# Performance work log

Measured on AMD Instinct MI355X. Metric: run time of the kernel, lower is better.

The kernel has to match this reference:

```python
import jax, jax.numpy as jnp
import numpy as np

BATCH, INPUT_DIM, HIDDEN_DIM, SEQ_LENGTH = 128, 256, 512, 1024


def setup_inputs() -> dict:
    key = jax.random.key(0)
    k1, k2, k3, k4, k5 = jax.random.split(key, 5)
    s = 1.0 / np.sqrt(HIDDEN_DIM)  # PyTorch GRU init: U(-1/sqrt(H), 1/sqrt(H))
    return {
        "input_features": jax.random.normal(k1, (BATCH, INPUT_DIM), dtype=jnp.float32),
        # PyTorch layout: rows stacked as [reset; update; new], each [H, *]
        "w_ih": jax.random.uniform(k2, (3 * HIDDEN_DIM, INPUT_DIM), minval=-s, maxval=s, dtype=jnp.float32),
        "w_hh": jax.random.uniform(k3, (3 * HIDDEN_DIM, HIDDEN_DIM), minval=-s, maxval=s, dtype=jnp.float32),
        "b_ih": jax.random.uniform(k4, (3 * HIDDEN_DIM,), minval=-s, maxval=s, dtype=jnp.float32),
        "b_hh": jax.random.uniform(k5, (3 * HIDDEN_DIM,), minval=-s, maxval=s, dtype=jnp.float32),
    }


def reference(input_features, w_ih, w_hh, b_ih, b_hh):
    # Decoder: run the GRU cell SEQ_LENGTH times with the SAME input x each
    # step, feeding back the hidden state; collect per-step outputs.
    B = input_features.shape[0]
    H = w_hh.shape[1]
    # Input contribution is constant across steps -> compute once.  [B, 3H]
    gi = input_features @ w_ih.T + b_ih
    gi_r, gi_z, gi_n = jnp.split(gi, 3, axis=-1)

    def step(h, _):
        gh = h @ w_hh.T + b_hh  # [B, 3H]
        gh_r, gh_z, gh_n = jnp.split(gh, 3, axis=-1)
        r = jax.nn.sigmoid(gi_r + gh_r)
        z = jax.nn.sigmoid(gi_z + gh_z)
        n = jnp.tanh(gi_n + r * gh_n)
        h_new = (1.0 - z) * n + z * h
        return h_new, h_new

    h0 = jnp.zeros((B, H), dtype=input_features.dtype)
    _, outs = jax.lax.scan(step, h0, None, length=SEQ_LENGTH)  # [S, B, H]
    return jnp.transpose(outs, (1, 0, 2))  # [B, SEQ_LENGTH, H]
```

## Files before the change

### kernel.cpp

```cpp
#include <hip/hip_runtime.h>
#include <hip/hip_bf16.h>
#include <stdint.h>


constexpr int SEQ = 1024;
constexpr int BATCH = 128;
constexpr int IND = 256;
constexpr int HD = 512;
constexpr int BG = 8;
constexpr int HG = 32;
constexpr int ROWS = BATCH / BG;
constexpr int NT = 3;
constexpr int RING_D = 8;
constexpr int SLOT_DW = BATCH * HD / 2;
constexpr size_t RING_BYTES = (size_t)RING_D * SLOT_DW * 4;

using frag16 = __attribute__((ext_vector_type(8))) short;
using f32x4  = __attribute__((ext_vector_type(4))) float;
using u32x4  = __attribute__((ext_vector_type(4))) unsigned;

__device__ __forceinline__ float sigmoid_f(float x) {
    return 1.f / (1.f + __expf(-x));
}
__device__ __forceinline__ float tanh_f(float x) {
    float e = __expf(2.f * x);
    return 1.f - 2.f / (e + 1.f);
}
__device__ __forceinline__ short f2bf(float x) {
    return (short)__bfloat16_as_ushort(__float2bfloat16(x));
}

__global__ __launch_bounds__(64, 1) void gru_kernel(
    const float* __restrict__ x,
    const float* __restrict__ w_ih,
    const float* __restrict__ w_hh,
    const float* __restrict__ b_ih,
    const float* __restrict__ b_hh,
    unsigned* __restrict__ ring,
    float* __restrict__ out)
{
    const int lane = threadIdx.x;
    const int bg = blockIdx.x & 7;
    const int hg = blockIdx.x >> 3;
    const int b0 = bg * ROWS;
    const int c0 = hg * 16;
    const int nlo = lane & 15;
    const int quad = lane >> 4;

    int gcol[NT];
    gcol[0] = c0 + nlo;
    gcol[1] = HD + c0 + nlo;
    gcol[2] = 2 * HD + c0 + nlo;

    __shared__ frag16 ldsB[NT * 16 * 64];
#pragma unroll
    for (int t = 0; t < NT; ++t) {
        for (int kc = 0; kc < 16; ++kc) {
            const float* src = w_hh + (size_t)gcol[t] * HD + kc * 32 + quad * 8;
            float4 v0 = *(const float4*)src;
            float4 v1 = *(const float4*)(src + 4);
            frag16 f;
            f[0] = f2bf(v0.x); f[1] = f2bf(v0.y); f[2] = f2bf(v0.z); f[3] = f2bf(v0.w);
            f[4] = f2bf(v1.x); f[5] = f2bf(v1.y); f[6] = f2bf(v1.z); f[7] = f2bf(v1.w);
            ldsB[(t * 16 + kc) * 64 + lane] = f;
        }
    }

    float gi[NT][4];
    float bhn = b_hh[gcol[2]];
#pragma unroll
    for (int t = 0; t < NT; ++t) {
        float bi = b_ih[gcol[t]] + ((t < 2) ? b_hh[gcol[t]] : 0.f);
#pragma unroll
        for (int r = 0; r < 4; ++r) gi[t][r] = bi;
    }
    for (int r = 0; r < 4; ++r) {
        const float4* xr = (const float4*)(x + (size_t)(b0 + quad * 4 + r) * IND);
        for (int kc = 0; kc < IND / 4; ++kc) {
            float4 xv = xr[kc];
#pragma unroll
            for (int t = 0; t < NT; ++t) {
                float4 wv = ((const float4*)(w_ih + (size_t)gcol[t] * IND))[kc];
                gi[t][r] += xv.x * wv.x + xv.y * wv.y + xv.z * wv.z + xv.w * wv.w;
            }
        }
    }

    const size_t arow_byte = (size_t)(b0 + nlo) * (HD * 2) + quad * 16;

    float hreg[4] = {0.f, 0.f, 0.f, 0.f};

    for (int s = 0; s < SEQ; ++s) {
        f32x4 C[NT];
#pragma unroll
        for (int t = 0; t < NT; ++t) C[t] = (f32x4){0.f, 0.f, 0.f, 0.f};

        if (s > 0) {
            const char* lrow =
                (const char*)(ring + ((s - 1) & (RING_D - 1)) * SLOT_DW) + arow_byte;
            u32x4 raw[16];
            unsigned vmask = 0u;
            do {
#pragma unroll
                for (int kc = 0; kc < 16; ++kc) {
                    if (!(vmask & (1u << kc))) {
                        asm volatile("global_load_dwordx4 %0, %1, off sc0 sc1"
                                     : "=v"(raw[kc]) : "v"(lrow + kc * 64) : "memory");
                    }
                }
                asm volatile("s_waitcnt vmcnt(0)" ::: "memory");
                __builtin_amdgcn_sched_barrier(0);
#pragma unroll
                for (int kc = 0; kc < 16; ++kc) {
                    if (!(vmask & (1u << kc))) {
                        unsigned orr = raw[kc][0] | raw[kc][1] | raw[kc][2] | raw[kc][3];
                        if (__ballot((orr & 0x40004000u) == 0u) == ~0ull)
                            vmask |= (1u << kc);
                    }
                }
            } while (vmask != 0xFFFFu);
#pragma unroll
            for (int kc = 0; kc < 16; ++kc) {
                union { u32x4 u; frag16 f; } cv;
                cv.u = raw[kc];
#pragma unroll
                for (int t = 0; t < NT; ++t) {
                    frag16 bfr = ldsB[(t * 16 + kc) * 64 + lane];
                    C[t] = __builtin_amdgcn_mfma_f32_16x16x32_bf16(cv.f, bfr, C[t], 0, 0, 0);
                }
            }
        }

        unsigned* wslot = ring + (s & (RING_D - 1)) * SLOT_DW;
        unsigned* rslot = ring + ((s + 2) & (RING_D - 1)) * SLOT_DW;
        float hn[4];
#pragma unroll
        for (int r = 0; r < 4; ++r) {
            float gr  = gi[0][r] + C[0][r];
            float gz  = gi[1][r] + C[1][r];
            float ghn = C[2][r] + bhn;
            float rr = sigmoid_f(gr);
            float zz = sigmoid_f(gz);
            float nn = tanh_f(gi[2][r] + rr * ghn);
            hn[r] = (1.f - zz) * nn + zz * hreg[r];
            hreg[r] = hn[r];
            unsigned own = (unsigned)(unsigned short)f2bf(hn[r]);
            unsigned other = (unsigned)__shfl_xor((int)own, 1);
            if ((lane & 1) == 0) {
                int row = b0 + quad * 4 + r;
                unsigned idx = (unsigned)(row * HD + (c0 + nlo)) >> 1;
                __hip_atomic_store(wslot + idx, own | (other << 16),
                                   __ATOMIC_RELAXED, __HIP_MEMORY_SCOPE_SYSTEM);
            }
        }
#pragma unroll
        for (int r = 0; r < 4; ++r) {
            if ((lane & 1) == 0) {
                int row = b0 + quad * 4 + r;
                unsigned idx = (unsigned)(row * HD + (c0 + nlo)) >> 1;
                __hip_atomic_store(rslot + idx, 0xFFFFFFFFu,
                                   __ATOMIC_RELAXED, __HIP_MEMORY_SCOPE_SYSTEM);
            }
        }
#pragma unroll
        for (int r = 0; r < 4; ++r) {
            int row = b0 + quad * 4 + r;
            __builtin_nontemporal_store(
                hn[r], out + (size_t)row * (SEQ * HD) + (size_t)s * HD + (c0 + nlo));
        }
    }
}

extern "C" void kernel_launch(void* const* d_in, const int* in_sizes, int n_in,
                              void* d_out, int out_size, void* d_ws, size_t ws_size,
                              hipStream_t stream) {
    (void)in_sizes; (void)n_in; (void)out_size; (void)ws_size;
    const float* x    = (const float*)d_in[0];
    const float* w_ih = (const float*)d_in[1];
    const float* w_hh = (const float*)d_in[2];
    const float* b_ih = (const float*)d_in[3];
    const float* b_hh = (const float*)d_in[4];

    unsigned* ring = (unsigned*)d_ws;
    hipMemsetAsync(ring, 0xFF, RING_BYTES, stream);
    gru_kernel<<<BG * HG, 64, 0, stream>>>(x, w_ih, w_hh, b_ih, b_hh, ring,
                                           (float*)d_out);
}
```

Before: 2.974 ms.

## Overlap ring polling with MFMA and defer output/sentinel stores off critical path

Restructures the per-step spin-wait on the shared hidden-state ring. Loads are issued once up front, then each polled chunk that is ready is consumed immediately by its MFMAs while only the not-yet-ready chunks are reloaded. The sentinel reset of a future ring slot and the output store for the previous step move into the window where loads are in flight, taking them off the step's critical path. Readiness is combined with a shuffle-AND reduction instead of a ballot per chunk. The sentinel now resets slot s+1 rather than s+2, which narrows the margin against blocks that fall behind, and the extra bookkeeping adds to the polling loop.

```diff
diff --git a/kernel.cpp b/kernel.cpp
--- a/kernel.cpp
+++ b/kernel.cpp
@@ -99,41 +99,75 @@
             const char* lrow =
                 (const char*)(ring + ((s - 1) & (RING_D - 1)) * SLOT_DW) + arow_byte;
             u32x4 raw[16];
-            unsigned vmask = 0u;
+#pragma unroll
+            for (int kc = 0; kc < 16; ++kc)
+                asm volatile("global_load_dwordx4 %0, %1, off sc0 sc1"
+                             : "=&v"(raw[kc]) : "v"(lrow + kc * 64) : "memory");
+            {
+                unsigned* rslot = ring + ((s + 1) & (RING_D - 1)) * SLOT_DW;
+#pragma unroll
+                for (int r = 0; r < 4; ++r) {
+                    if ((lane & 1) == 0) {
+                        int row = b0 + quad * 4 + r;
+                        unsigned idx = (unsigned)(row * HD + (c0 + nlo)) >> 1;
+                        __hip_atomic_store(rslot + idx, 0xFFFFFFFFu,
+                                           __ATOMIC_RELAXED, __HIP_MEMORY_SCOPE_SYSTEM);
+                    }
+                }
+#pragma unroll
+                for (int r = 0; r < 4; ++r) {
+                    int row = b0 + quad * 4 + r;
+                    __builtin_nontemporal_store(
+                        hreg[r],
+                        out + (size_t)row * (SEQ * HD) + (size_t)(s - 1) * HD + (c0 + nlo));
+                }
+            }
+            unsigned vmask = 0;
+            int round = 0;
             do {
-#pragma unroll
-                for (int kc = 0; kc < 16; ++kc) {
-                    if (!(vmask & (1u << kc))) {
-                        asm volatile("global_load_dwordx4 %0, %1, off sc0 sc1"
-                                     : "=v"(raw[kc]) : "v"(lrow + kc * 64) : "memory");
-                    }
-                }
-                asm volatile("s_waitcnt vmcnt(0)" ::: "memory");
+                if (round == 0)
+                    asm volatile("s_waitcnt vmcnt(8)" ::: "memory");
+                else
+                    asm volatile("s_waitcnt vmcnt(0)" ::: "memory");
+                ++round;
                 __builtin_amdgcn_sched_barrier(0);
+                unsigned ok = 0;
 #pragma unroll
                 for (int kc = 0; kc < 16; ++kc) {
                     if (!(vmask & (1u << kc))) {
                         unsigned orr = raw[kc][0] | raw[kc][1] | raw[kc][2] | raw[kc][3];
-                        if (__ballot((orr & 0x40004000u) == 0u) == ~0ull)
-                            vmask |= (1u << kc);
+                        ok |= ((orr & 0x40004000u) == 0u) ? (1u << kc) : 0u;
                     }
                 }
+#pragma unroll
+                for (int d = 1; d < 64; d <<= 1)
+                    ok &= (unsigned)__shfl_xor((int)ok, d);
+                unsigned newv = __builtin_amdgcn_readfirstlane(ok & ~vmask) & 0xFFFFu;
+                unsigned still = 0xFFFFu & ~(vmask | newv);
+#pragma unroll
+                for (int kc = 0; kc < 16; ++kc) {
+                    if (still & (1u << kc))
+                        asm volatile("global_load_dwordx4 %0, %1, off sc0 sc1"
+                                     : "=&v"(raw[kc]) : "v"(lrow + kc * 64) : "memory");
+                }
+#pragma unroll
+                for (int kc = 0; kc < 16; ++kc) {
+                    if (newv & (1u << kc)) {
+                        union { u32x4 u; frag16 f; } cv;
+                        cv.u = raw[kc];
+#pragma unroll
+                        for (int t = 0; t < NT; ++t) {
+                            frag16 bfr = ldsB[(t * 16 + kc) * 64 + lane];
+                            C[t] = __builtin_amdgcn_mfma_f32_16x16x32_bf16(cv.f, bfr,
+                                                                           C[t], 0, 0, 0);
+                        }
+                    }
+                }
+                vmask |= newv;
             } while (vmask != 0xFFFFu);
-#pragma unroll
-            for (int kc = 0; kc < 16; ++kc) {
-                union { u32x4 u; frag16 f; } cv;
-                cv.u = raw[kc];
-#pragma unroll
-                for (int t = 0; t < NT; ++t) {
-                    frag16 bfr = ldsB[(t * 16 + kc) * 64 + lane];
-                    C[t] = __builtin_amdgcn_mfma_f32_16x16x32_bf16(cv.f, bfr, C[t], 0, 0, 0);
-                }
-            }
         }
 
         unsigned* wslot = ring + (s & (RING_D - 1)) * SLOT_DW;
-        unsigned* rslot = ring + ((s + 2) & (RING_D - 1)) * SLOT_DW;
-        float hn[4];
 #pragma unroll
         for (int r = 0; r < 4; ++r) {
             float gr  = gi[0][r] + C[0][r];
@@ -142,9 +176,9 @@
             float rr = sigmoid_f(gr);
             float zz = sigmoid_f(gz);
             float nn = tanh_f(gi[2][r] + rr * ghn);
-            hn[r] = (1.f - zz) * nn + zz * hreg[r];
-            hreg[r] = hn[r];
-            unsigned own = (unsigned)(unsigned short)f2bf(hn[r]);
+            float hn = (1.f - zz) * nn + zz * hreg[r];
+            hreg[r] = hn;
+            unsigned own = (unsigned)(unsigned short)f2bf(hn);
             unsigned other = (unsigned)__shfl_xor((int)own, 1);
             if ((lane & 1) == 0) {
                 int row = b0 + quad * 4 + r;
@@ -153,21 +187,14 @@
                                    __ATOMIC_RELAXED, __HIP_MEMORY_SCOPE_SYSTEM);
             }
         }
-#pragma unroll
-        for (int r = 0; r < 4; ++r) {
-            if ((lane & 1) == 0) {
-                int row = b0 + quad * 4 + r;
-                unsigned idx = (unsigned)(row * HD + (c0 + nlo)) >> 1;
-                __hip_atomic_store(rslot + idx, 0xFFFFFFFFu,
-                                   __ATOMIC_RELAXED, __HIP_MEMORY_SCOPE_SYSTEM);
-            }
-        }
-#pragma unroll
-        for (int r = 0; r < 4; ++r) {
-            int row = b0 + quad * 4 + r;
-            __builtin_nontemporal_store(
-                hn[r], out + (size_t)row * (SEQ * HD) + (size_t)s * HD + (c0 + nlo));
-        }
+    }
+
+#pragma unroll
+    for (int r = 0; r < 4; ++r) {
+        int row = b0 + quad * 4 + r;
+        __builtin_nontemporal_store(
+            hreg[r],
+            out + (size_t)row * (SEQ * HD) + (size_t)(SEQ - 1) * HD + (c0 + nlo));
     }
 }
 
```

Measured after the change: 5.366 ms. 1.8x slower.

## Pair two waves per block and share polled hidden-state halves through LDS

Applied to the files above, without the earlier changes.

Blocks now hold two wavefronts that cover adjacent 16-column slices. Each wave polls only half of the K chunks of the previous hidden state from the global ring and exchanges its half with the other wave through a double-buffered LDS buffer and __syncthreads. This halves the per-wave global polling traffic and the number of blocks contending on the ring. In exchange it adds a block-level barrier every step and doubles LDS use.

```diff
diff --git a/kernel.cpp b/kernel.cpp
--- a/kernel.cpp
+++ b/kernel.cpp
@@ -8,7 +8,7 @@
 constexpr int IND = 256;
 constexpr int HD = 512;
 constexpr int BG = 8;
-constexpr int HG = 32;
+constexpr int CG = 16;
 constexpr int ROWS = BATCH / BG;
 constexpr int NT = 3;
 constexpr int RING_D = 8;
@@ -30,7 +30,7 @@
     return (short)__bfloat16_as_ushort(__float2bfloat16(x));
 }
 
-__global__ __launch_bounds__(64, 1) void gru_kernel(
+__global__ __launch_bounds__(128, 1) void gru_kernel(
     const float* __restrict__ x,
     const float* __restrict__ w_ih,
     const float* __restrict__ w_hh,
@@ -39,11 +39,13 @@
     unsigned* __restrict__ ring,
     float* __restrict__ out)
 {
-    const int lane = threadIdx.x;
+    const int tid  = threadIdx.x;
+    const int wv   = tid >> 6;
+    const int lane = tid & 63;
     const int bg = blockIdx.x & 7;
-    const int hg = blockIdx.x >> 3;
+    const int cg = blockIdx.x >> 3;
     const int b0 = bg * ROWS;
-    const int c0 = hg * 16;
+    const int c0 = cg * 32 + wv * 16;
     const int nlo = lane & 15;
     const int quad = lane >> 4;
 
@@ -52,7 +54,10 @@
     gcol[1] = HD + c0 + nlo;
     gcol[2] = 2 * HD + c0 + nlo;
 
-    __shared__ frag16 ldsB[NT * 16 * 64];
+    __shared__ frag16 ldsB[2][NT * 16 * 64];
+    __shared__ u32x4  abuf[2][16 * 64];
+    frag16* myB = &ldsB[wv][0];
+
 #pragma unroll
     for (int t = 0; t < NT; ++t) {
         for (int kc = 0; kc < 16; ++kc) {
@@ -62,7 +67,7 @@
             frag16 f;
             f[0] = f2bf(v0.x); f[1] = f2bf(v0.y); f[2] = f2bf(v0.z); f[3] = f2bf(v0.w);
             f[4] = f2bf(v1.x); f[5] = f2bf(v1.y); f[6] = f2bf(v1.z); f[7] = f2bf(v1.w);
-            ldsB[(t * 16 + kc) * 64 + lane] = f;
+            myB[(t * 16 + kc) * 64 + lane] = f;
         }
     }
 
@@ -80,13 +85,15 @@
             float4 xv = xr[kc];
 #pragma unroll
             for (int t = 0; t < NT; ++t) {
-                float4 wv = ((const float4*)(w_ih + (size_t)gcol[t] * IND))[kc];
-                gi[t][r] += xv.x * wv.x + xv.y * wv.y + xv.z * wv.z + xv.w * wv.w;
+                float4 wv4 = ((const float4*)(w_ih + (size_t)gcol[t] * IND))[kc];
+                gi[t][r] += xv.x * wv4.x + xv.y * wv4.y + xv.z * wv4.z + xv.w * wv4.w;
             }
         }
     }
 
     const size_t arow_byte = (size_t)(b0 + nlo) * (HD * 2) + quad * 16;
+    const int kbase = wv * 8;
+    const int obase = 8 - kbase;
 
     float hreg[4] = {0.f, 0.f, 0.f, 0.f};
 
@@ -98,34 +105,56 @@
         if (s > 0) {
             const char* lrow =
                 (const char*)(ring + ((s - 1) & (RING_D - 1)) * SLOT_DW) + arow_byte;
-            u32x4 raw[16];
+            u32x4 rown[8];
+            u32x4 roth[8];
             unsigned vmask = 0u;
             do {
 #pragma unroll
-                for (int kc = 0; kc < 16; ++kc) {
-                    if (!(vmask & (1u << kc))) {
+                for (int i = 0; i < 8; ++i) {
+                    if (!(vmask & (1u << i))) {
                         asm volatile("global_load_dwordx4 %0, %1, off sc0 sc1"
-                                     : "=v"(raw[kc]) : "v"(lrow + kc * 64) : "memory");
+                                     : "=v"(rown[i])
+                                     : "v"(lrow + (kbase + i) * 64) : "memory");
                     }
                 }
                 asm volatile("s_waitcnt vmcnt(0)" ::: "memory");
                 __builtin_amdgcn_sched_barrier(0);
 #pragma unroll
-                for (int kc = 0; kc < 16; ++kc) {
-                    if (!(vmask & (1u << kc))) {
-                        unsigned orr = raw[kc][0] | raw[kc][1] | raw[kc][2] | raw[kc][3];
+                for (int i = 0; i < 8; ++i) {
+                    if (!(vmask & (1u << i))) {
+                        unsigned orr = rown[i][0] | rown[i][1] | rown[i][2] | rown[i][3];
                         if (__ballot((orr & 0x40004000u) == 0u) == ~0ull)
-                            vmask |= (1u << kc);
+                            vmask |= (1u << i);
                     }
                 }
-            } while (vmask != 0xFFFFu);
-#pragma unroll
-            for (int kc = 0; kc < 16; ++kc) {
+            } while (vmask != 0xFFu);
+            u32x4* ab = &abuf[s & 1][0];
+#pragma unroll
+            for (int i = 0; i < 8; ++i)
+                ab[(kbase + i) * 64 + lane] = rown[i];
+            __syncthreads();
+#pragma unroll
+            for (int i = 0; i < 8; ++i)
+                roth[i] = ab[(obase + i) * 64 + lane];
+#pragma unroll
+            for (int i = 0; i < 8; ++i) {
                 union { u32x4 u; frag16 f; } cv;
-                cv.u = raw[kc];
+                cv.u = rown[i];
+                const int kc = kbase + i;
 #pragma unroll
                 for (int t = 0; t < NT; ++t) {
-                    frag16 bfr = ldsB[(t * 16 + kc) * 64 + lane];
+                    frag16 bfr = myB[(t * 16 + kc) * 64 + lane];
+                    C[t] = __builtin_amdgcn_mfma_f32_16x16x32_bf16(cv.f, bfr, C[t], 0, 0, 0);
+                }
+            }
+#pragma unroll
+            for (int i = 0; i < 8; ++i) {
+                union { u32x4 u; frag16 f; } cv;
+                cv.u = roth[i];
+                const int kc = obase + i;
+#pragma unroll
+                for (int t = 0; t < NT; ++t) {
+                    frag16 bfr = myB[(t * 16 + kc) * 64 + lane];
                     C[t] = __builtin_amdgcn_mfma_f32_16x16x32_bf16(cv.f, bfr, C[t], 0, 0, 0);
                 }
             }
@@ -183,6 +212,6 @@
 
     unsigned* ring = (unsigned*)d_ws;
     hipMemsetAsync(ring, 0xFF, RING_BYTES, stream);
-    gru_kernel<<<BG * HG, 64, 0, stream>>>(x, w_ih, w_hh, b_ih, b_hh, ring,
-                                           (float*)d_out);
-}
+    gru_kernel<<<BG * CG, 128, 0, stream>>>(x, w_ih, w_hh, b_ih, b_hh, ring,
+                                            (float*)d_out);
+}
```

New measurement: 3.787 ms. +27.3%, slower.

## Give each workgroup two 16-column hidden tiles, halving the persistent grid

Applied to the files above, without the earlier changes.

Each single-wave workgroup now owns 32 hidden columns (two 16-wide tiles per gate) instead of 16, so the grid shrinks from 256 to 128 workgroups. Each wave reads the shared bf16 hidden-state row fragments from the ring once and reuses them for six MFMA accumulators instead of three. This halves the number of participants polling the global ring each step and doubles the reuse of each loaded A fragment. In exchange each wave does twice the MFMA and elementwise work on the serial per-step critical path, and uses more LDS and registers.

```diff
diff --git a/kernel.cpp b/kernel.cpp
--- a/kernel.cpp
+++ b/kernel.cpp
@@ -8,9 +8,9 @@
 constexpr int IND = 256;
 constexpr int HD = 512;
 constexpr int BG = 8;
-constexpr int HG = 32;
+constexpr int CG = 16;
 constexpr int ROWS = BATCH / BG;
-constexpr int NT = 3;
+constexpr int NT = 6;
 constexpr int RING_D = 8;
 constexpr int SLOT_DW = BATCH * HD / 2;
 constexpr size_t RING_BYTES = (size_t)RING_D * SLOT_DW * 4;
@@ -41,16 +41,18 @@
 {
     const int lane = threadIdx.x;
     const int bg = blockIdx.x & 7;
-    const int hg = blockIdx.x >> 3;
+    const int cg = blockIdx.x >> 3;
     const int b0 = bg * ROWS;
-    const int c0 = hg * 16;
+    const int c0 = cg * 32;
     const int nlo = lane & 15;
     const int quad = lane >> 4;
 
     int gcol[NT];
-    gcol[0] = c0 + nlo;
-    gcol[1] = HD + c0 + nlo;
-    gcol[2] = 2 * HD + c0 + nlo;
+#pragma unroll
+    for (int g = 0; g < 3; ++g)
+#pragma unroll
+        for (int ct = 0; ct < 2; ++ct)
+            gcol[g * 2 + ct] = g * HD + c0 + ct * 16 + nlo;
 
     __shared__ frag16 ldsB[NT * 16 * 64];
 #pragma unroll
@@ -67,10 +69,10 @@
     }
 
     float gi[NT][4];
-    float bhn = b_hh[gcol[2]];
+    float bhn2[2] = {b_hh[gcol[4]], b_hh[gcol[5]]};
 #pragma unroll
     for (int t = 0; t < NT; ++t) {
-        float bi = b_ih[gcol[t]] + ((t < 2) ? b_hh[gcol[t]] : 0.f);
+        float bi = b_ih[gcol[t]] + ((t < 4) ? b_hh[gcol[t]] : 0.f);
 #pragma unroll
         for (int r = 0; r < 4; ++r) gi[t][r] = bi;
     }
@@ -88,7 +90,11 @@
 
     const size_t arow_byte = (size_t)(b0 + nlo) * (HD * 2) + quad * 16;
 
-    float hreg[4] = {0.f, 0.f, 0.f, 0.f};
+    float hreg[2][4];
+#pragma unroll
+    for (int ct = 0; ct < 2; ++ct)
+#pragma unroll
+        for (int r = 0; r < 4; ++r) hreg[ct][r] = 0.f;
 
     for (int s = 0; s < SEQ; ++s) {
         f32x4 C[NT];
@@ -133,40 +139,54 @@
 
         unsigned* wslot = ring + (s & (RING_D - 1)) * SLOT_DW;
         unsigned* rslot = ring + ((s + 2) & (RING_D - 1)) * SLOT_DW;
-        float hn[4];
-#pragma unroll
-        for (int r = 0; r < 4; ++r) {
-            float gr  = gi[0][r] + C[0][r];
-            float gz  = gi[1][r] + C[1][r];
-            float ghn = C[2][r] + bhn;
-            float rr = sigmoid_f(gr);
-            float zz = sigmoid_f(gz);
-            float nn = tanh_f(gi[2][r] + rr * ghn);
-            hn[r] = (1.f - zz) * nn + zz * hreg[r];
-            hreg[r] = hn[r];
-            unsigned own = (unsigned)(unsigned short)f2bf(hn[r]);
-            unsigned other = (unsigned)__shfl_xor((int)own, 1);
-            if ((lane & 1) == 0) {
+        float hn[2][4];
+#pragma unroll
+        for (int ct = 0; ct < 2; ++ct) {
+#pragma unroll
+            for (int r = 0; r < 4; ++r) {
+                float gr  = gi[0 + ct][r] + C[0 + ct][r];
+                float gz  = gi[2 + ct][r] + C[2 + ct][r];
+                float ghn = C[4 + ct][r] + bhn2[ct];
+                float rr = sigmoid_f(gr);
+                float zz = sigmoid_f(gz);
+                float nn = tanh_f(gi[4 + ct][r] + rr * ghn);
+                float h = (1.f - zz) * nn + zz * hreg[ct][r];
+                hn[ct][r] = h;
+                hreg[ct][r] = h;
+                unsigned own = (unsigned)(unsigned short)f2bf(h);
+                unsigned other = (unsigned)__shfl_xor((int)own, 1);
+                if ((lane & 1) == 0) {
+                    int row = b0 + quad * 4 + r;
+                    int col = c0 + ct * 16 + nlo;
+                    unsigned idx = (unsigned)(row * HD + col) >> 1;
+                    __hip_atomic_store(wslot + idx, own | (other << 16),
+                                       __ATOMIC_RELAXED, __HIP_MEMORY_SCOPE_SYSTEM);
+                }
+            }
+        }
+#pragma unroll
+        for (int ct = 0; ct < 2; ++ct) {
+#pragma unroll
+            for (int r = 0; r < 4; ++r) {
+                if ((lane & 1) == 0) {
+                    int row = b0 + quad * 4 + r;
+                    int col = c0 + ct * 16 + nlo;
+                    unsigned idx = (unsigned)(row * HD + col) >> 1;
+                    __hip_atomic_store(rslot + idx, 0xFFFFFFFFu,
+                                       __ATOMIC_RELAXED, __HIP_MEMORY_SCOPE_SYSTEM);
+                }
+            }
+        }
+#pragma unroll
+        for (int ct = 0; ct < 2; ++ct) {
+#pragma unroll
+            for (int r = 0; r < 4; ++r) {
                 int row = b0 + quad * 4 + r;
-                unsigned idx = (unsigned)(row * HD + (c0 + nlo)) >> 1;
-                __hip_atomic_store(wslot + idx, own | (other << 16),
-                                   __ATOMIC_RELAXED, __HIP_MEMORY_SCOPE_SYSTEM);
-            }
-        }
-#pragma unroll
-        for (int r = 0; r < 4; ++r) {
-            if ((lane & 1) == 0) {
-                int row = b0 + quad * 4 + r;
-                unsigned idx = (unsigned)(row * HD + (c0 + nlo)) >> 1;
-                __hip_atomic_store(rslot + idx, 0xFFFFFFFFu,
-                                   __ATOMIC_RELAXED, __HIP_MEMORY_SCOPE_SYSTEM);
-            }
-        }
-#pragma unroll
-        for (int r = 0; r < 4; ++r) {
-            int row = b0 + quad * 4 + r;
-            __builtin_nontemporal_store(
-                hn[r], out + (size_t)row * (SEQ * HD) + (size_t)s * HD + (c0 + nlo));
+                int col = c0 + ct * 16 + nlo;
+                __builtin_nontemporal_store(
+                    hn[ct][r],
+                    out + (size_t)row * (SEQ * HD) + (size_t)s * HD + col);
+            }
         }
     }
 }
@@ -183,6 +203,6 @@
 
     unsigned* ring = (unsigned*)d_ws;
     hipMemsetAsync(ring, 0xFF, RING_BYTES, stream);
-    gru_kernel<<<BG * HG, 64, 0, stream>>>(x, w_ih, w_hh, b_ih, b_hh, ring,
+    gru_kernel<<<BG * CG, 64, 0, stream>>>(x, w_ih, w_hh, b_ih, b_hh, ring,
                                            (float*)d_out);
 }
```

Result: slower. 4.257 ms (+43.2%).
